# Performance work log

Hardware: AMD Instinct MI355X
Metric: run time of the kernel (lower is better)

## Reference

```python
import jax, jax.numpy as jnp
import numpy as np

B_ = 2; L_ = 4096; D_MODEL = 1024; D_INNER = 2048; D_STATE = 128
N_HEADS = 32; HEADDIM = 64; D_CONV = 4; CHUNK = 64
CONV_DIM = D_INNER + 2 * D_STATE
EPS = 1e-5


def silu(x):
    return x * jax.nn.sigmoid(x)


def segsum(x):
    # x: (..., T) -> (..., T, T) stable segment sums; exp() gives 1-semiseparable matrix
    T = x.shape[-1]
    xe = jnp.broadcast_to(x[..., None], x.shape + (T,))  # (..., T, T)
    lower = jnp.tril(jnp.ones((T, T), bool), -1)
    xs = jnp.cumsum(jnp.where(lower, xe, 0.0), axis=-2)
    incl = jnp.tril(jnp.ones((T, T), bool), 0)
    return jnp.where(incl, xs, -jnp.inf)


def ssd(x, A, Bm, Cm):
    # x: (b, l, h, p); A: (b, l, h); Bm/Cm: (b, l, n) (single shared head, as in module)
    b, l, h, p = x.shape
    c = l // CHUNK
    x = x.reshape(b, c, CHUNK, h, p)
    A = A.reshape(b, c, CHUNK, h).transpose(0, 3, 1, 2)  # (b, h, c, l)
    Bm = Bm.reshape(b, c, CHUNK, D_STATE)
    Cm = Cm.reshape(b, c, CHUNK, D_STATE)
    A_cumsum = jnp.cumsum(A, axis=-1)                    # (b, h, c, l)
    Lmat = jnp.exp(segsum(A))                            # (b, h, c, l, l)
    # intra-chunk (diagonal blocks)
    Y_diag = jnp.einsum('bcln,bcsn,bhcls,bcshp->bclhp', Cm, Bm, Lmat, x)
    # per-chunk states
    decay_states = jnp.exp(A_cumsum[:, :, :, -1:] - A_cumsum)  # (b, h, c, l)
    states = jnp.einsum('bcln,bhcl,bclhp->bchpn', Bm, decay_states, x)
    init = jnp.zeros_like(states[:, :1])
    states = jnp.concatenate([init, states], axis=1)     # (b, c+1, h, p, n)
    A_last = jnp.pad(A_cumsum[:, :, :, -1], ((0, 0), (0, 0), (1, 0)))  # (b, h, c+1)
    decay_chunk = jnp.exp(segsum(A_last))                # (b, h, c+1, c+1)
    new_states = jnp.einsum('bhzc,bchpn->bzhpn', decay_chunk, states)
    states_prev = new_states[:, :-1]                     # (b, c, h, p, n)
    state_decay_out = jnp.exp(A_cumsum)
    Y_off = jnp.einsum('bcln,bchpn,bhcl->bclhp', Cm, states_prev, state_decay_out)
    return (Y_diag + Y_off).reshape(b, l, h, p)


def setup_inputs() -> dict:
    key = jax.random.key(0)
    ks = jax.random.split(key, 9)
    u = jax.random.normal(ks[0], (B_, L_, D_MODEL), jnp.float32)
    W_in = jax.random.normal(ks[1], (2 * D_INNER + 2 * D_STATE + N_HEADS, D_MODEL), jnp.float32) * (D_MODEL ** -0.5)
    conv_w = jax.random.normal(ks[2], (CONV_DIM, 1, D_CONV), jnp.float32) * 0.2
    conv_b = jax.random.normal(ks[3], (CONV_DIM,), jnp.float32) * 0.02
    dt_bias = jax.random.normal(ks[4], (N_HEADS,), jnp.float32) * 0.1
    A_log = jnp.log(jax.random.uniform(ks[5], (N_HEADS,), jnp.float32, 1.0, 16.0))
    D_param = jax.random.normal(ks[6], (N_HEADS,), jnp.float32) * 0.5
    norm_w = jnp.ones((D_INNER,), jnp.float32)
    W_out = jax.random.normal(ks[7], (D_MODEL, D_INNER), jnp.float32) * (D_INNER ** -0.5)
    return dict(u=u, W_in=W_in, conv_w=conv_w, conv_b=conv_b, dt_bias=dt_bias,
                A_log=A_log, D_param=D_param, norm_w=norm_w, W_out=W_out)


def mamba_forward(u, W_in, conv_w, conv_b, dt_bias, A_log, D_param, norm_w, W_out):
    b, l, _ = u.shape
    zxbcdt = u @ W_in.T                                  # (b, l, 2*di+2*ds+h)
    z = zxbcdt[..., :D_INNER]
    xBC = zxbcdt[..., D_INNER:D_INNER + CONV_DIM]
    dt = zxbcdt[..., D_INNER + CONV_DIM:]
    dt = jax.nn.softplus(dt + dt_bias)                   # (b, l, h)
    # causal depthwise conv1d
    xc = jnp.transpose(xBC, (0, 2, 1))                   # (b, conv_dim, l)
    xc = jax.lax.conv_general_dilated(xc, conv_w, (1,), [(D_CONV - 1, 0)],
                                      feature_group_count=CONV_DIM,
                                      dimension_numbers=('NCH', 'OIH', 'NCH'))
    xc = xc + conv_b[None, :, None]
    xBC = silu(jnp.transpose(xc, (0, 2, 1)))             # (b, l, conv_dim)
    x = xBC[..., :D_INNER]
    Bc = xBC[..., D_INNER:D_INNER + D_STATE]
    Cc = xBC[..., D_INNER + D_STATE:]
    x = x.reshape(b, l, N_HEADS, HEADDIM)
    A = -jnp.exp(A_log)                                  # (h,)
    Y = ssd(x * dt[..., None], A * dt, Bc, Cc)           # (b, l, h, p)
    y = Y + x * D_param[:, None]
    y = y.reshape(b, l, D_INNER)
    # gated RMSNorm
    y = y * silu(z)
    y = y * jax.lax.rsqrt(jnp.mean(y * y, axis=-1, keepdims=True) + EPS) * norm_w
    return y @ W_out.T


def reference(u, W_in, conv_w, conv_b, dt_bias, A_log, D_param, norm_w, W_out):
    return mamba_forward(u, W_in, conv_w, conv_b, dt_bias, A_log, D_param, norm_w, W_out)
```

## Files before the change

### kernel.cpp

```cpp
#include <hip/hip_runtime.h>
#include <hip/hip_bf16.h>
#include <math.h>

#define B_    2
#define L_    4096
#define DM    1024
#define DI    2048
#define DS    128
#define NH    32
#define HD    64
#define CHUNK 64
#define NC    (L_/CHUNK)
#define CD    (DI + 2*DS)
#define ROWS  (B_*L_)
#define NOUT  (2*DI + 2*DS + NH)
#define NPAD2 4608

typedef __attribute__((ext_vector_type(4))) float f32x4;
typedef __attribute__((ext_vector_type(8))) __bf16 bf16x8;
typedef __attribute__((ext_vector_type(4))) short s16x4;
typedef __attribute__((ext_vector_type(8))) short s16x8;

__global__ __launch_bounds__(256) void k_f32_to_bf16(const float* __restrict__ s, __bf16* __restrict__ d, int n4) {
    int i = blockIdx.x * 256 + threadIdx.x;
    if (i < n4) {
        f32x4 v = *(const f32x4*)(s + (size_t)i * 4);
        s16x4 o;
#pragma unroll
        for (int q = 0; q < 4; q++) o[q] = __builtin_bit_cast(short, (__bf16)v[q]);
        *(s16x4*)(d + (size_t)i * 4) = o;
    }
}

__global__ __launch_bounds__(256) void k_convert_pad(const float* __restrict__ s, __bf16* __restrict__ d, int nsrc4, int ndst4) {
    int i = blockIdx.x * 256 + threadIdx.x;
    if (i < ndst4) {
        s16x4 o = {0, 0, 0, 0};
        if (i < nsrc4) {
            f32x4 v = *(const f32x4*)(s + (size_t)i * 4);
#pragma unroll
            for (int q = 0; q < 4; q++) o[q] = __builtin_bit_cast(short, (__bf16)v[q]);
        }
        *(s16x4*)(d + (size_t)i * 4) = o;
    }
}

__device__ __forceinline__ void stage_half(const __bf16* __restrict__ G, int ldg, int grow0, int kt,
                                           char* lds, int ldsoff, int tid, int wave) {
#pragma unroll
    for (int issue = 0; issue < 2; issue++) {
        int o   = issue * 8192 + tid * 16;
        int row = o >> 7;
        int cb  = (o & 127) ^ ((row & 7) << 4);
        const __bf16* src = G + (size_t)(grow0 + row) * ldg + kt + (cb >> 1);
        char* ldsbase = lds + ldsoff + issue * 8192 + wave * 1024;
        __builtin_amdgcn_global_load_lds((const __attribute__((address_space(1))) void*)src,
                                         (__attribute__((address_space(3))) void*)ldsbase,
                                         16, 0, 0);
    }
}

__device__ __forceinline__ bf16x8 rdfrag(const char* lds, int ldsoff, int r, int ks, int lane) {
    int logical = r * 128 + ks * 64 + ((lane >> 4) << 4);
    int phys    = logical ^ ((r & 7) << 4);
    return *(const bf16x8*)(lds + ldsoff + phys);
}

#define MFMA_CLUSTER(AF, BF, ACC)                                                         \
    __builtin_amdgcn_s_setprio(1);                                                       \
    _Pragma("unroll")                                                                    \
    for (int fm = 0; fm < 4; fm++)                                                       \
        _Pragma("unroll")                                                                \
        for (int fn = 0; fn < 2; fn++)                                                   \
            _Pragma("unroll")                                                            \
            for (int ks = 0; ks < 2; ks++)                                               \
                ACC[fm][fn] = __builtin_amdgcn_mfma_f32_16x16x32_bf16(AF[fm][ks], BF[fn][ks], ACC[fm][fn], 0, 0, 0); \
    __builtin_amdgcn_s_setprio(0);

__device__ __forceinline__ void gemm128x256_core(const __bf16* __restrict__ Ag, const __bf16* __restrict__ Bg,
                                                 int K, int m0, int n0, char* lds, f32x4 acc[4][4]) {
    const int tid = threadIdx.x, wave = tid >> 6, lane = tid & 63;
    const int wm = wave >> 2, wn = wave & 3, lrow = lane & 15;
    const int KT = K >> 6;
    const int brow = wn * 64;
    const int bhalf = 16384 + ((brow >> 7) << 14);
    const int brl = brow & 127;

    for (int t = 0; t < KT; t++) {
        const int kt = t << 6;
        stage_half(Ag, K, m0,       kt, lds, 0,     tid, wave);
        stage_half(Bg, K, n0,       kt, lds, 16384, tid, wave);
        stage_half(Bg, K, n0 + 128, kt, lds, 32768, tid, wave);
        asm volatile("s_waitcnt vmcnt(0)" ::: "memory");
        __builtin_amdgcn_s_barrier();
        bf16x8 a[4][2];
#pragma unroll
        for (int fm = 0; fm < 4; fm++)
#pragma unroll
            for (int ks = 0; ks < 2; ks++)
                a[fm][ks] = rdfrag(lds, 0, wm * 64 + fm * 16 + lrow, ks, lane);
        __builtin_amdgcn_s_setprio(1);
#pragma unroll
        for (int fn = 0; fn < 4; fn++) {
            bf16x8 b0 = rdfrag(lds, bhalf, brl + fn * 16 + lrow, 0, lane);
            bf16x8 b1 = rdfrag(lds, bhalf, brl + fn * 16 + lrow, 1, lane);
#pragma unroll
            for (int fm = 0; fm < 4; fm++) {
                acc[fm][fn] = __builtin_amdgcn_mfma_f32_16x16x32_bf16(a[fm][0], b0, acc[fm][fn], 0, 0, 0);
                acc[fm][fn] = __builtin_amdgcn_mfma_f32_16x16x32_bf16(a[fm][1], b1, acc[fm][fn], 0, 0, 0);
            }
        }
        __builtin_amdgcn_s_setprio(0);
        __builtin_amdgcn_s_barrier();
    }
}

__device__ __forceinline__ void gemm256x128_core(const __bf16* __restrict__ Ag, const __bf16* __restrict__ Bg,
                                                 int K, int m0, int n0, char* lds, f32x4 acc[8][2]) {
    const int tid = threadIdx.x, wave = tid >> 6, lane = tid & 63;
    const int wmq = wave >> 2, wnq = wave & 3, lrow = lane & 15;
    const int KT = K >> 6;
    const int aoff = wmq * 16384;

    auto stage_tile = [&](int t, int p) {
        const int kt = t << 6;
        stage_half(Ag, K, m0,       kt, lds, p * 49152,         tid, wave);
        stage_half(Ag, K, m0 + 128, kt, lds, p * 49152 + 16384, tid, wave);
        stage_half(Bg, K, n0,       kt, lds, p * 49152 + 32768, tid, wave);
    };
    stage_tile(0, 0);
    asm volatile("s_waitcnt vmcnt(0)" ::: "memory");
    __builtin_amdgcn_s_barrier();

    bf16x8 ra[4][2], rb[2][2];
#pragma unroll
    for (int fm = 0; fm < 4; fm++)
#pragma unroll
        for (int ks = 0; ks < 2; ks++)
            ra[fm][ks] = rdfrag(lds, aoff, fm * 16 + lrow, ks, lane);
#pragma unroll
    for (int fn = 0; fn < 2; fn++)
#pragma unroll
        for (int ks = 0; ks < 2; ks++)
            rb[fn][ks] = rdfrag(lds, 32768, wnq * 32 + fn * 16 + lrow, ks, lane);

    for (int t = 0; t < KT; t++) {
        const int p = t & 1, pn = p ^ 1;
        const bool dsg = (t + 1 < KT);
        if (dsg) {
            stage_half(Ag, K, m0,       (t + 1) << 6, lds, pn * 49152,         tid, wave);
            stage_half(Ag, K, m0 + 128, (t + 1) << 6, lds, pn * 49152 + 16384, tid, wave);
        }
        {
            f32x4 (*a0)[2] = &acc[0];
            MFMA_CLUSTER(ra, rb, a0);
        }
#pragma unroll
        for (int fm = 0; fm < 4; fm++)
#pragma unroll
            for (int ks = 0; ks < 2; ks++)
                ra[fm][ks] = rdfrag(lds, p * 49152 + aoff, 64 + fm * 16 + lrow, ks, lane);
        if (dsg) stage_half(Bg, K, n0, (t + 1) << 6, lds, pn * 49152 + 32768, tid, wave);
        {
            f32x4 (*a1)[2] = &acc[4];
            MFMA_CLUSTER(ra, rb, a1);
        }
        asm volatile("s_waitcnt vmcnt(0)" ::: "memory");
        __builtin_amdgcn_s_barrier();
        if (dsg) {
#pragma unroll
            for (int fm = 0; fm < 4; fm++)
#pragma unroll
                for (int ks = 0; ks < 2; ks++)
                    ra[fm][ks] = rdfrag(lds, pn * 49152 + aoff, fm * 16 + lrow, ks, lane);
#pragma unroll
            for (int fn = 0; fn < 2; fn++)
#pragma unroll
                for (int ks = 0; ks < 2; ks++)
                    rb[fn][ks] = rdfrag(lds, pn * 49152 + 32768, wnq * 32 + fn * 16 + lrow, ks, lane);
        }
    }
}

__global__ __launch_bounds__(512, 4) void k_gemm1(const __bf16* __restrict__ ubf, const __bf16* __restrict__ wibf,
                                                  __bf16* __restrict__ zbuf, __bf16* __restrict__ xbcraw,
                                                  float* __restrict__ dtbuf, const float* __restrict__ dt_bias) {
    extern __shared__ char lds[];
    f32x4 acc[4][4];
    f32x4 z4 = {0.f, 0.f, 0.f, 0.f};
#pragma unroll
    for (int i = 0; i < 4; i++)
#pragma unroll
        for (int j = 0; j < 4; j++) acc[i][j] = z4;

    int bid = blockIdx.x;
    int wg  = (bid & 7) * 144 + (bid >> 3);
    int m0  = (wg / 18) * 128;
    int n0  = (wg % 18) * 256;
    gemm128x256_core(ubf, wibf, DM, m0, n0, lds, acc);

    const int lane = threadIdx.x & 63, wave = threadIdx.x >> 6;
    const int wm = wave >> 2, wn = wave & 3;
    const int gm_base = m0 + wm * 64 + ((lane >> 4) << 2);
    const int gn_base = n0 + wn * 64 + (lane & 15);
#pragma unroll
    for (int fm = 0; fm < 4; fm++) {
        const int gmb = gm_base + fm * 16;
#pragma unroll
        for (int fn = 0; fn < 4; fn++) {
            const int gn = gn_base + fn * 16;
            if (gn < DI) {
#pragma unroll
                for (int r = 0; r < 4; r++)
                    zbuf[(size_t)(gmb + r) * DI + gn] = (__bf16)acc[fm][fn][r];
            } else if (gn < DI + CD) {
#pragma unroll
                for (int r = 0; r < 4; r++)
                    xbcraw[(size_t)(gmb + r) * CD + (gn - DI)] = (__bf16)acc[fm][fn][r];
            } else if (gn < NOUT) {
                const int hh = gn - (DI + CD);
                const float bb = dt_bias[hh];
#pragma unroll
                for (int r = 0; r < 4; r++) {
                    float x = acc[fm][fn][r] + bb;
                    float sp = (x > 20.f) ? x : log1pf(__expf(x));
                    dtbuf[(size_t)(gmb + r) * NH + hh] = sp;
                }
            }
        }
    }
}

__global__ __launch_bounds__(512, 2) void k_gemm2(const __bf16* __restrict__ ybf, const __bf16* __restrict__ wobf,
                                                  float* __restrict__ out) {
    extern __shared__ char lds[];
    f32x4 acc[8][2];
    f32x4 z4 = {0.f, 0.f, 0.f, 0.f};
#pragma unroll
    for (int i = 0; i < 8; i++)
#pragma unroll
        for (int j = 0; j < 2; j++) acc[i][j] = z4;

    int bid = blockIdx.x;
    int wg  = (bid & 7) * 32 + (bid >> 3);
    int m0  = (wg / 8) * 256;
    int n0  = (wg % 8) * 128;
    gemm256x128_core(ybf, wobf, DI, m0, n0, lds, acc);

    const int lane = threadIdx.x & 63, wave = threadIdx.x >> 6;
    const int wmq = wave >> 2, wnq = wave & 3;
#pragma unroll
    for (int fm = 0; fm < 8; fm++) {
        const int gmb = m0 + wmq * 128 + fm * 16 + ((lane >> 4) << 2);
#pragma unroll
        for (int fn = 0; fn < 2; fn++) {
            const int gn = n0 + wnq * 32 + fn * 16 + (lane & 15);
#pragma unroll
            for (int r = 0; r < 4; r++)
                out[(size_t)(gmb + r) * DM + gn] = acc[fm][fn][r];
        }
    }
}

__global__ __launch_bounds__(256) void k_conv(const __bf16* __restrict__ xbcraw, const float* __restrict__ conv_w,
                                              const float* __restrict__ conv_b, __bf16* __restrict__ xconv) {
    __shared__ float wsh[256 * 4];
    __shared__ float bsh[256];
    const int tid  = threadIdx.x;
    const int gsub = tid & 31;
    const int roct = tid >> 5;
    const int ch_base_blk = blockIdx.x * 256;
    *(f32x4*)&wsh[tid * 4] = *(const f32x4*)&conv_w[ch_base_blk * 4 + tid * 4];
    bsh[tid] = conv_b[ch_base_blk + tid];
    __syncthreads();

    const int ch0  = ch_base_blk + gsub * 8;
    const int row0 = (blockIdx.y * 8 + roct) * 8;
    const int l0   = row0 & (L_ - 1);
    const __bf16* src = xbcraw + (size_t)row0 * CD + ch0;

    s16x8 rr[11];
#pragma unroll
    for (int j = 0; j < 11; j++) {
        int ll = l0 - 3 + j;
        if (ll >= 0) rr[j] = *(const s16x8*)(src + (size_t)(j - 3) * CD);
        else         rr[j] = (s16x8){0, 0, 0, 0, 0, 0, 0, 0};
    }

    const int chl = gsub * 8;
    float w[8][4], bias[8];
#pragma unroll
    for (int j = 0; j < 8; j++) {
        bias[j] = bsh[chl + j];
#pragma unroll
        for (int k = 0; k < 4; k++) w[j][k] = wsh[(chl + j) * 4 + k];
    }

    __bf16* dst = xconv + (size_t)row0 * CD + ch0;
#pragma unroll
    for (int orow = 0; orow < 8; orow++) {
        float a[8];
#pragma unroll
        for (int j = 0; j < 8; j++) a[j] = bias[j];
#pragma unroll
        for (int k = 0; k < 4; k++) {
            s16x8 v = rr[orow + k];
#pragma unroll
            for (int j = 0; j < 8; j++)
                a[j] += w[j][k] * (float)__builtin_bit_cast(__bf16, (short)v[j]);
        }
        s16x8 o;
#pragma unroll
        for (int j = 0; j < 8; j++)
            o[j] = __builtin_bit_cast(short, (__bf16)(a[j] * __builtin_amdgcn_rcpf(1.f + __expf(-a[j]))));
        *(s16x8*)(dst + (size_t)orow * CD) = o;
    }
}

__global__ __launch_bounds__(256) void k_cbt(const __bf16* __restrict__ xconv, float* __restrict__ cbt) {
    const int c = blockIdx.x, b = blockIdx.y;
    const int tid = threadIdx.x, wv = tid >> 6, lane = tid & 63;
    const int lrow = lane & 15, lko = (lane >> 4) * 8;
    __shared__ __align__(16) __bf16 Csh[64 * 136];
    __shared__ __align__(16) __bf16 Bsh[64 * 136];
    const size_t rowbase = (size_t)b * L_ + c * CHUNK;
#pragma unroll
    for (int q = 0; q < 32; q++) {
        int i = q * 2 + (wv >> 1);
        int n = (wv & 1) * 64 + lane;
        const __bf16* base = xconv + (rowbase + i) * CD + DI;
        Bsh[i * 136 + n] = base[n];
        Csh[i * 136 + n] = base[DS + n];
    }
    __syncthreads();
    f32x4 acc[4];
    f32x4 z4 = {0.f, 0.f, 0.f, 0.f};
#pragma unroll
    for (int jt = 0; jt < 4; jt++) acc[jt] = z4;
#pragma unroll
    for (int ks = 0; ks < 4; ks++) {
        bf16x8 a = *(const bf16x8*)&Csh[(wv * 16 + lrow) * 136 + ks * 32 + lko];
#pragma unroll
        for (int jt = 0; jt < 4; jt++) {
            bf16x8 bb = *(const bf16x8*)&Bsh[(jt * 16 + lrow) * 136 + ks * 32 + lko];
            acc[jt] = __builtin_amdgcn_mfma_f32_16x16x32_bf16(a, bb, acc[jt], 0, 0, 0);
        }
    }
    float* o = cbt + (size_t)(b * NC + c) * 4096;
#pragma unroll
    for (int jt = 0; jt < 4; jt++)
#pragma unroll
        for (int r = 0; r < 4; r++) {
            int i = wv * 16 + (lane >> 4) * 4 + r;
            int j = jt * 16 + lrow;
            o[i * 64 + j] = acc[jt][r];
        }
}

__global__ __launch_bounds__(256) void k_ssd_a(const __bf16* __restrict__ xconv, const float* __restrict__ dtbuf,
                                               const float* __restrict__ cbt, const float* __restrict__ A_log,
                                               __bf16* __restrict__ ybuf, __bf16* __restrict__ states,
                                               float* __restrict__ asum, const float* __restrict__ D_param) {
    const int h = blockIdx.x, c = blockIdx.y, b = blockIdx.z;
    const int tid = threadIdx.x, wv = tid >> 6, lane = tid & 63;
    const int lrow = lane & 15, lko = (lane >> 4) * 8;
    __shared__ __align__(16) __bf16 xT[64 * 72];
    __shared__ __align__(16) __bf16 xsc[64 * 72];
    __shared__ __align__(16) __bf16 BT[128 * 72];
    __shared__ __align__(16) __bf16 Ms[64 * 72];
    __shared__ float dts[64], cum[64];

    const float Ah = -__expf(A_log[h]);
    const size_t rowbase = (size_t)b * L_ + c * CHUNK;

    float dtv = 0.f;
    if (wv == 0) { dtv = dtbuf[(rowbase + lane) * NH + h]; dts[lane] = dtv; }
#pragma unroll
    for (int q = 0; q < 16; q++) {
        int i = q * 4 + wv;
        xT[lane * 72 + i] = xconv[(rowbase + i) * CD + h * HD + lane];
    }
#pragma unroll
    for (int q = 0; q < 32; q++) {
        int i = q * 2 + (wv >> 1);
        int n = (wv & 1) * 64 + lane;
        BT[n * 72 + i] = xconv[(rowbase + i) * CD + DI + n];
    }
    if (wv == 0) {
        float v = Ah * dtv;
#pragma unroll
        for (int o = 1; o < 64; o <<= 1) { float t = __shfl_up(v, o); if (lane >= o) v += t; }
        cum[lane] = v;
        if (lane == 63) asum[(b * NC + c) * NH + h] = v;
    }
    __syncthreads();

    const float cum63 = cum[63];
    const float Dh = D_param[h];
    const float* cbt_bc = cbt + (size_t)(b * NC + c) * 4096;
#pragma unroll
    for (int q = 0; q < 16; q++) {
        int i = q * 4 + wv, j = lane;
        float cumi = cum[i];
        float m = 0.f;
        if (j <= i) m = cbt_bc[i * 64 + j] * __expf(cumi - cum[j]) * dts[j];
        if (j == i) m += Dh;
        Ms[i * 72 + j] = (__bf16)m;
        float dcfi = __expf(cum63 - cumi) * dts[i];
        xsc[lane * 72 + i] = (__bf16)((float)xT[lane * 72 + i] * dcfi);
    }
    __syncthreads();

    f32x4 z4 = {0.f, 0.f, 0.f, 0.f};
    {
        f32x4 accY[4];
#pragma unroll
        for (int pt = 0; pt < 4; pt++) accY[pt] = z4;
#pragma unroll
        for (int ks = 0; ks < 2; ks++) {
            bf16x8 a = *(const bf16x8*)&Ms[(wv * 16 + lrow) * 72 + ks * 32 + lko];
#pragma unroll
            for (int pt = 0; pt < 4; pt++) {
                bf16x8 bb = *(const bf16x8*)&xT[(pt * 16 + lrow) * 72 + ks * 32 + lko];
                accY[pt] = __builtin_amdgcn_mfma_f32_16x16x32_bf16(a, bb, accY[pt], 0, 0, 0);
            }
        }
#pragma unroll
        for (int pt = 0; pt < 4; pt++)
#pragma unroll
            for (int r = 0; r < 4; r++) {
                int i = wv * 16 + (lane >> 4) * 4 + r;
                int p = pt * 16 + lrow;
                ybuf[(rowbase + i) * DI + h * HD + p] = (__bf16)accY[pt][r];
            }
    }
    {
        f32x4 accS[8];
#pragma unroll
        for (int nt = 0; nt < 8; nt++) accS[nt] = z4;
#pragma unroll
        for (int ks = 0; ks < 2; ks++) {
            bf16x8 a = *(const bf16x8*)&xsc[(wv * 16 + lrow) * 72 + ks * 32 + lko];
#pragma unroll
            for (int nt = 0; nt < 8; nt++) {
                bf16x8 bb = *(const bf16x8*)&BT[(nt * 16 + lrow) * 72 + ks * 32 + lko];
                accS[nt] = __builtin_amdgcn_mfma_f32_16x16x32_bf16(a, bb, accS[nt], 0, 0, 0);
            }
        }
        __bf16* sp = states + ((size_t)(b * NC + c) * NH + h) * 8192;
#pragma unroll
        for (int nt = 0; nt < 8; nt++)
#pragma unroll
            for (int r = 0; r < 4; r++) {
                int p = wv * 16 + (lane >> 4) * 4 + r;
                int n = nt * 16 + lrow;
                sp[p * 128 + n] = (__bf16)accS[nt][r];
            }
    }
}

__global__ __launch_bounds__(256) void k_scan(__bf16* __restrict__ states, const float* __restrict__ asum) {
    const int seg = blockIdx.x, h = blockIdx.y, b = blockIdx.z;
    __shared__ float efs[NC];
    if (threadIdx.x < NC) efs[threadIdx.x] = __expf(asum[(b * NC + threadIdx.x) * NH + h]);
    __syncthreads();
    const int e0 = seg * 1024 + threadIdx.x * 4;
    __bf16* base = states + ((size_t)(b * NC) * NH + h) * 8192 + e0;
    const size_t cs = (size_t)NH * 8192;
    float S[4] = {0.f, 0.f, 0.f, 0.f};
    s16x4 r0 = *(const s16x4*)(base);
    s16x4 r1 = *(const s16x4*)(base + cs);
    s16x4 r2 = *(const s16x4*)(base + 2 * cs);
    s16x4 r3;
#define SCAN_STEP(RV, CC)                                                                  \
    {                                                                                      \
        s16x4 o; float e = efs[CC];                                                        \
        _Pragma("unroll")                                                                  \
        for (int q = 0; q < 4; q++) {                                                      \
            float t = (float)__builtin_bit_cast(__bf16, (short)RV[q]);                     \
            o[q] = __builtin_bit_cast(short, (__bf16)S[q]);                                \
            S[q] = e * S[q] + t;                                                           \
        }                                                                                  \
        *(s16x4*)(base + (size_t)(CC) * cs) = o;                                           \
    }
    for (int c = 0; c < NC; c += 4) {
        r3 = *(const s16x4*)(base + (size_t)(c + 3) * cs);
        SCAN_STEP(r0, c);
        if (c + 4 < NC) r0 = *(const s16x4*)(base + (size_t)(c + 4) * cs);
        SCAN_STEP(r1, c + 1);
        if (c + 5 < NC) r1 = *(const s16x4*)(base + (size_t)(c + 5) * cs);
        SCAN_STEP(r2, c + 2);
        if (c + 6 < NC) r2 = *(const s16x4*)(base + (size_t)(c + 6) * cs);
        SCAN_STEP(r3, c + 3);
    }
#undef SCAN_STEP
}

__global__ __launch_bounds__(256) void k_ssd_b(const __bf16* __restrict__ xconv, const float* __restrict__ dtbuf,
                                               const __bf16* __restrict__ states, const float* __restrict__ A_log,
                                               __bf16* __restrict__ ybuf) {
    const int h = blockIdx.x, c = blockIdx.y, b = blockIdx.z;
    const int tid = threadIdx.x, wv = tid >> 6, lane = tid & 63;
    const int lrow = lane & 15, lko = (lane >> 4) * 8;
    __shared__ __align__(16) __bf16 Csh[64 * 136];
    __shared__ __align__(16) __bf16 Sps[64 * 136];
    __shared__ float cum[64];

    const float Ah = -__expf(A_log[h]);
    const size_t rowbase = (size_t)b * L_ + c * CHUNK;
    const __bf16* sp = states + ((size_t)(b * NC + c) * NH + h) * 8192;
#pragma unroll
    for (int q = 0; q < 32; q++) {
        int i = q * 2 + (wv >> 1);
        int n = (wv & 1) * 64 + lane;
        Csh[i * 136 + n] = xconv[(rowbase + i) * CD + DI + DS + n];
        Sps[i * 136 + n] = sp[i * 128 + n];
    }
    if (wv == 0) {
        float v = Ah * dtbuf[(rowbase + lane) * NH + h];
#pragma unroll
        for (int o = 1; o < 64; o <<= 1) { float t = __shfl_up(v, o); if (lane >= o) v += t; }
        cum[lane] = v;
    }
    __syncthreads();

    f32x4 acc[4];
    f32x4 z4 = {0.f, 0.f, 0.f, 0.f};
#pragma unroll
    for (int pt = 0; pt < 4; pt++) acc[pt] = z4;
#pragma unroll
    for (int ks = 0; ks < 4; ks++) {
        bf16x8 a = *(const bf16x8*)&Csh[(wv * 16 + lrow) * 136 + ks * 32 + lko];
#pragma unroll
        for (int pt = 0; pt < 4; pt++) {
            bf16x8 bb = *(const bf16x8*)&Sps[(pt * 16 + lrow) * 136 + ks * 32 + lko];
            acc[pt] = __builtin_amdgcn_mfma_f32_16x16x32_bf16(a, bb, acc[pt], 0, 0, 0);
        }
    }
#pragma unroll
    for (int r = 0; r < 4; r++) {
        int i = wv * 16 + (lane >> 4) * 4 + r;
        float ef = __expf(cum[i]);
#pragma unroll
        for (int pt = 0; pt < 4; pt++) {
            size_t idx = (rowbase + i) * DI + h * HD + pt * 16 + lrow;
            float y0 = (float)ybuf[idx];
            ybuf[idx] = (__bf16)(y0 + ef * acc[pt][r]);
        }
    }
}

__global__ __launch_bounds__(256) void k_gate_norm(const __bf16* __restrict__ ybuf, const __bf16* __restrict__ zbuf,
                                                   const float* __restrict__ norm_w, __bf16* __restrict__ ybf) {
    const int r = blockIdx.x;
    const int tid = threadIdx.x;
    const int col0 = tid * 8;
    s16x8 y8 = *(const s16x8*)(ybuf + (size_t)r * DI + col0);
    s16x8 z8 = *(const s16x8*)(zbuf + (size_t)r * DI + col0);
    float v[8];
    float ss = 0.f;
#pragma unroll
    for (int q = 0; q < 8; q++) {
        float y = (float)__builtin_bit_cast(__bf16, (short)y8[q]);
        float z = (float)__builtin_bit_cast(__bf16, (short)z8[q]);
        float g = z * __builtin_amdgcn_rcpf(1.f + __expf(-z));
        v[q] = y * g;
        ss += v[q] * v[q];
    }
#pragma unroll
    for (int o = 32; o > 0; o >>= 1) ss += __shfl_down(ss, o);
    __shared__ float wsum[4];
    __shared__ float rmss;
    if ((tid & 63) == 0) wsum[tid >> 6] = ss;
    __syncthreads();
    if (tid == 0) {
        float t = wsum[0] + wsum[1] + wsum[2] + wsum[3];
        rmss = rsqrtf(t / (float)DI + 1e-5f);
    }
    __syncthreads();
    float rm = rmss;
    s16x8 o8;
#pragma unroll
    for (int q = 0; q < 8; q++)
        o8[q] = __builtin_bit_cast(short, (__bf16)(v[q] * rm * norm_w[col0 + q]));
    *(s16x8*)(ybf + (size_t)r * DI + col0) = o8;
}

extern "C" void kernel_launch(void* const* d_in, const int* in_sizes, int n_in,
                              void* d_out, int out_size, void* d_ws, size_t ws_size,
                              hipStream_t stream) {
    const float* u       = (const float*)d_in[0];
    const float* W_in    = (const float*)d_in[1];
    const float* conv_w  = (const float*)d_in[2];
    const float* conv_b  = (const float*)d_in[3];
    const float* dt_bias = (const float*)d_in[4];
    const float* A_log   = (const float*)d_in[5];
    const float* D_param = (const float*)d_in[6];
    const float* norm_w  = (const float*)d_in[7];
    const float* W_out   = (const float*)d_in[8];
    float* out = (float*)d_out;

    constexpr size_t OFF_WOBF  = 0;
    constexpr size_t OFF_ZBUF  = 4194304;
    constexpr size_t OFF_DT    = 37748736;
    constexpr size_t OFF_ASUM  = 38797312;
    constexpr size_t OFF_XCONV = 38813696;
    constexpr size_t OFF_CBT   = 76562432;
    constexpr size_t OFF_BIG   = 78659584;
    constexpr size_t NEED      = 145768448;
    if (ws_size < NEED) return;

    char* ws = (char*)d_ws;
    __bf16* wobf   = (__bf16*)(ws + OFF_WOBF);
    __bf16* zbuf   = (__bf16*)(ws + OFF_ZBUF);
    float*  dtbuf  = (float*) (ws + OFF_DT);
    float*  asum   = (float*) (ws + OFF_ASUM);
    __bf16* xconv  = (__bf16*)(ws + OFF_XCONV);
    float*  cbt    = (float*) (ws + OFF_CBT);
    __bf16* ubf    = (__bf16*)(ws + OFF_BIG);
    __bf16* wibf   = (__bf16*)(ws + OFF_BIG + 16777216);
    __bf16* xbcraw = (__bf16*)(ws + OFF_BIG + 16777216 + 9437184);
    __bf16* states = (__bf16*)(ws + OFF_BIG);
    __bf16* ybf    = (__bf16*)(ws + OFF_XCONV);
    __bf16* ybuf   = (__bf16*)d_out;

    (void)hipFuncSetAttribute((const void*)k_gemm1, hipFuncAttributeMaxDynamicSharedMemorySize, 49152);
    (void)hipFuncSetAttribute((const void*)k_gemm2, hipFuncAttributeMaxDynamicSharedMemorySize, 98304);

    k_f32_to_bf16<<<(ROWS * DM / 4 + 255) / 256, 256, 0, stream>>>(u, ubf, ROWS * DM / 4);
    k_convert_pad<<<(NPAD2 * DM / 4 + 255) / 256, 256, 0, stream>>>(W_in, wibf, NOUT * DM / 4, NPAD2 * DM / 4);
    k_f32_to_bf16<<<(DM * DI / 4 + 255) / 256, 256, 0, stream>>>(W_out, wobf, DM * DI / 4);

    k_gemm1<<<1152, 512, 49152, stream>>>(ubf, wibf, zbuf, xbcraw, dtbuf, dt_bias);
    k_conv<<<dim3(9, 128), 256, 0, stream>>>(xbcraw, conv_w, conv_b, xconv);
    k_cbt<<<dim3(NC, B_), 256, 0, stream>>>(xconv, cbt);
    k_ssd_a<<<dim3(NH, NC, B_), 256, 0, stream>>>(xconv, dtbuf, cbt, A_log, ybuf, states, asum, D_param);
    k_scan<<<dim3(8, NH, B_), 256, 0, stream>>>(states, asum);
    k_ssd_b<<<dim3(NH, NC, B_), 256, 0, stream>>>(xconv, dtbuf, states, A_log, ybuf);
    k_gate_norm<<<ROWS, 256, 0, stream>>>(ybuf, zbuf, norm_w, ybf);
    k_gemm2<<<256, 512, 98304, stream>>>(ybf, wobf, out);
}
```

Before: 308.7 us.

## Loop eight heads per block in SSD kernels to reuse B/C tiles; merge conversions

k_ssd_a and k_ssd_b now each process eight heads per block in a loop. The shared B (and C) chunk tile is staged into LDS once and reused across heads instead of being reloaded 32 times per chunk. The three fp32-to-bf16 conversion launches are merged into a single kernel to cut launch overhead. In exchange, the SSD grids shrink from 4096 to 512 blocks, and the per-head work inside each block is serialized with extra barriers, which lowers parallelism and latency hiding on a large GPU.

```diff
diff --git a/kernel.cpp b/kernel.cpp
--- a/kernel.cpp
+++ b/kernel.cpp
@@ -21,28 +21,33 @@
 typedef __attribute__((ext_vector_type(4))) short s16x4;
 typedef __attribute__((ext_vector_type(8))) short s16x8;
 
-__global__ __launch_bounds__(256) void k_f32_to_bf16(const float* __restrict__ s, __bf16* __restrict__ d, int n4) {
+__global__ __launch_bounds__(256) void k_convert_all(const float* __restrict__ u, const float* __restrict__ W_in,
+                                                     const float* __restrict__ W_out, __bf16* __restrict__ ubf,
+                                                     __bf16* __restrict__ wibf, __bf16* __restrict__ wobf) {
     int i = blockIdx.x * 256 + threadIdx.x;
-    if (i < n4) {
-        f32x4 v = *(const f32x4*)(s + (size_t)i * 4);
-        s16x4 o;
+    const int QU  = ROWS * DM / 4;
+    const int QWI = NPAD2 * DM / 4;
+    const int QWO = DM * DI / 4;
+    const float* s = nullptr;
+    __bf16* d;
+    bool zero = false;
+    if (i < QU) {
+        s = u + (size_t)i * 4; d = ubf + (size_t)i * 4;
+    } else if (i < QU + QWI) {
+        int j = i - QU;
+        d = wibf + (size_t)j * 4;
+        if (j < NOUT * DM / 4) s = W_in + (size_t)j * 4; else zero = true;
+    } else if (i < QU + QWI + QWO) {
+        int j = i - QU - QWI;
+        s = W_out + (size_t)j * 4; d = wobf + (size_t)j * 4;
+    } else return;
+    s16x4 o = {0, 0, 0, 0};
+    if (!zero) {
+        f32x4 v = *(const f32x4*)s;
 #pragma unroll
         for (int q = 0; q < 4; q++) o[q] = __builtin_bit_cast(short, (__bf16)v[q]);
-        *(s16x4*)(d + (size_t)i * 4) = o;
-    }
-}
-
-__global__ __launch_bounds__(256) void k_convert_pad(const float* __restrict__ s, __bf16* __restrict__ d, int nsrc4, int ndst4) {
-    int i = blockIdx.x * 256 + threadIdx.x;
-    if (i < ndst4) {
-        s16x4 o = {0, 0, 0, 0};
-        if (i < nsrc4) {
-            f32x4 v = *(const f32x4*)(s + (size_t)i * 4);
-#pragma unroll
-            for (int q = 0; q < 4; q++) o[q] = __builtin_bit_cast(short, (__bf16)v[q]);
-        }
-        *(s16x4*)(d + (size_t)i * 4) = o;
-    }
+    }
+    *(s16x4*)d = o;
 }
 
 __device__ __forceinline__ void stage_half(const __bf16* __restrict__ G, int ldg, int grow0, int kt,
@@ -361,7 +366,7 @@
                                                const float* __restrict__ cbt, const float* __restrict__ A_log,
                                                __bf16* __restrict__ ybuf, __bf16* __restrict__ states,
                                                float* __restrict__ asum, const float* __restrict__ D_param) {
-    const int h = blockIdx.x, c = blockIdx.y, b = blockIdx.z;
+    const int hg = blockIdx.x, c = blockIdx.y, b = blockIdx.z;
     const int tid = threadIdx.x, wv = tid >> 6, lane = tid & 63;
     const int lrow = lane & 15, lko = (lane >> 4) * 8;
     __shared__ __align__(16) __bf16 xT[64 * 72];
@@ -370,92 +375,96 @@
     __shared__ __align__(16) __bf16 Ms[64 * 72];
     __shared__ float dts[64], cum[64];
 
-    const float Ah = -__expf(A_log[h]);
     const size_t rowbase = (size_t)b * L_ + c * CHUNK;
-
-    float dtv = 0.f;
-    if (wv == 0) { dtv = dtbuf[(rowbase + lane) * NH + h]; dts[lane] = dtv; }
-#pragma unroll
-    for (int q = 0; q < 16; q++) {
-        int i = q * 4 + wv;
-        xT[lane * 72 + i] = xconv[(rowbase + i) * CD + h * HD + lane];
-    }
 #pragma unroll
     for (int q = 0; q < 32; q++) {
         int i = q * 2 + (wv >> 1);
         int n = (wv & 1) * 64 + lane;
         BT[n * 72 + i] = xconv[(rowbase + i) * CD + DI + n];
     }
-    if (wv == 0) {
-        float v = Ah * dtv;
-#pragma unroll
-        for (int o = 1; o < 64; o <<= 1) { float t = __shfl_up(v, o); if (lane >= o) v += t; }
-        cum[lane] = v;
-        if (lane == 63) asum[(b * NC + c) * NH + h] = v;
-    }
-    __syncthreads();
-
-    const float cum63 = cum[63];
-    const float Dh = D_param[h];
     const float* cbt_bc = cbt + (size_t)(b * NC + c) * 4096;
-#pragma unroll
-    for (int q = 0; q < 16; q++) {
-        int i = q * 4 + wv, j = lane;
-        float cumi = cum[i];
-        float m = 0.f;
-        if (j <= i) m = cbt_bc[i * 64 + j] * __expf(cumi - cum[j]) * dts[j];
-        if (j == i) m += Dh;
-        Ms[i * 72 + j] = (__bf16)m;
-        float dcfi = __expf(cum63 - cumi) * dts[i];
-        xsc[lane * 72 + i] = (__bf16)((float)xT[lane * 72 + i] * dcfi);
-    }
-    __syncthreads();
-
     f32x4 z4 = {0.f, 0.f, 0.f, 0.f};
-    {
-        f32x4 accY[4];
-#pragma unroll
-        for (int pt = 0; pt < 4; pt++) accY[pt] = z4;
-#pragma unroll
-        for (int ks = 0; ks < 2; ks++) {
-            bf16x8 a = *(const bf16x8*)&Ms[(wv * 16 + lrow) * 72 + ks * 32 + lko];
-#pragma unroll
-            for (int pt = 0; pt < 4; pt++) {
-                bf16x8 bb = *(const bf16x8*)&xT[(pt * 16 + lrow) * 72 + ks * 32 + lko];
-                accY[pt] = __builtin_amdgcn_mfma_f32_16x16x32_bf16(a, bb, accY[pt], 0, 0, 0);
+
+    for (int hh = 0; hh < 8; hh++) {
+        const int h = hg * 8 + hh;
+        const float Ah = -__expf(A_log[h]);
+        const float Dh = D_param[h];
+#pragma unroll
+        for (int q = 0; q < 16; q++) {
+            int i = q * 4 + wv;
+            xT[lane * 72 + i] = xconv[(rowbase + i) * CD + h * HD + lane];
+        }
+        if (wv == 0) {
+            float dtv = dtbuf[(rowbase + lane) * NH + h];
+            dts[lane] = dtv;
+            float v = Ah * dtv;
+#pragma unroll
+            for (int o = 1; o < 64; o <<= 1) { float t = __shfl_up(v, o); if (lane >= o) v += t; }
+            cum[lane] = v;
+            if (lane == 63) asum[(b * NC + c) * NH + h] = v;
+        }
+        __syncthreads();
+
+        const float cum63 = cum[63];
+#pragma unroll
+        for (int q = 0; q < 16; q++) {
+            int i = q * 4 + wv, j = lane;
+            float cumi = cum[i];
+            float m = 0.f;
+            if (j <= i) m = cbt_bc[i * 64 + j] * __expf(cumi - cum[j]) * dts[j];
+            if (j == i) m += Dh;
+            Ms[i * 72 + j] = (__bf16)m;
+            float dcfi = __expf(cum63 - cumi) * dts[i];
+            xsc[lane * 72 + i] = (__bf16)((float)xT[lane * 72 + i] * dcfi);
+        }
+        __syncthreads();
+
+        {
+            f32x4 accY[4];
+#pragma unroll
+            for (int pt = 0; pt < 4; pt++) accY[pt] = z4;
+#pragma unroll
+            for (int ks = 0; ks < 2; ks++) {
+                bf16x8 a = *(const bf16x8*)&Ms[(wv * 16 + lrow) * 72 + ks * 32 + lko];
+#pragma unroll
+                for (int pt = 0; pt < 4; pt++) {
+                    bf16x8 bb = *(const bf16x8*)&xT[(pt * 16 + lrow) * 72 + ks * 32 + lko];
+                    accY[pt] = __builtin_amdgcn_mfma_f32_16x16x32_bf16(a, bb, accY[pt], 0, 0, 0);
+                }
             }
-        }
-#pragma unroll
-        for (int pt = 0; pt < 4; pt++)
-#pragma unroll
-            for (int r = 0; r < 4; r++) {
-                int i = wv * 16 + (lane >> 4) * 4 + r;
-                int p = pt * 16 + lrow;
-                ybuf[(rowbase + i) * DI + h * HD + p] = (__bf16)accY[pt][r];
+#pragma unroll
+            for (int pt = 0; pt < 4; pt++)
+#pragma unroll
+                for (int r = 0; r < 4; r++) {
+                    int i = wv * 16 + (lane >> 4) * 4 + r;
+                    int p = pt * 16 + lrow;
+                    ybuf[(rowbase + i) * DI + h * HD + p] = (__bf16)accY[pt][r];
+                }
+        }
+        {
+            f32x4 accS[8];
+#pragma unroll
+            for (int nt = 0; nt < 8; nt++) accS[nt] = z4;
+#pragma unroll
+            for (int ks = 0; ks < 2; ks++) {
+                bf16x8 a = *(const bf16x8*)&xsc[(wv * 16 + lrow) * 72 + ks * 32 + lko];
+#pragma unroll
+                for (int nt = 0; nt < 8; nt++) {
+                    bf16x8 bb = *(const bf16x8*)&BT[(nt * 16 + lrow) * 72 + ks * 32 + lko];
+                    accS[nt] = __builtin_amdgcn_mfma_f32_16x16x32_bf16(a, bb, accS[nt], 0, 0, 0);
+                }
             }
-    }
-    {
-        f32x4 accS[8];
-#pragma unroll
-        for (int nt = 0; nt < 8; nt++) accS[nt] = z4;
-#pragma unroll
-        for (int ks = 0; ks < 2; ks++) {
-            bf16x8 a = *(const bf16x8*)&xsc[(wv * 16 + lrow) * 72 + ks * 32 + lko];
-#pragma unroll
-            for (int nt = 0; nt < 8; nt++) {
-                bf16x8 bb = *(const bf16x8*)&BT[(nt * 16 + lrow) * 72 + ks * 32 + lko];
-                accS[nt] = __builtin_amdgcn_mfma_f32_16x16x32_bf16(a, bb, accS[nt], 0, 0, 0);
-            }
-        }
-        __bf16* sp = states + ((size_t)(b * NC + c) * NH + h) * 8192;
-#pragma unroll
-        for (int nt = 0; nt < 8; nt++)
-#pragma unroll
-            for (int r = 0; r < 4; r++) {
-                int p = wv * 16 + (lane >> 4) * 4 + r;
-                int n = nt * 16 + lrow;
-                sp[p * 128 + n] = (__bf16)accS[nt][r];
-            }
+            __bf16* sp = states + ((size_t)(b * NC + c) * NH + h) * 8192;
+#pragma unroll
+            for (int nt = 0; nt < 8; nt++)
+#pragma unroll
+                for (int r = 0; r < 4; r++) {
+                    int p = wv * 16 + (lane >> 4) * 4 + r;
+                    int n = nt * 16 + lrow;
+                    sp[p * 128 + n] = (__bf16)accS[nt][r];
+                }
+        }
+        __syncthreads();
     }
 }
 
@@ -499,54 +508,64 @@
 __global__ __launch_bounds__(256) void k_ssd_b(const __bf16* __restrict__ xconv, const float* __restrict__ dtbuf,
                                                const __bf16* __restrict__ states, const float* __restrict__ A_log,
                                                __bf16* __restrict__ ybuf) {
-    const int h = blockIdx.x, c = blockIdx.y, b = blockIdx.z;
+    const int hg = blockIdx.x, c = blockIdx.y, b = blockIdx.z;
     const int tid = threadIdx.x, wv = tid >> 6, lane = tid & 63;
     const int lrow = lane & 15, lko = (lane >> 4) * 8;
     __shared__ __align__(16) __bf16 Csh[64 * 136];
     __shared__ __align__(16) __bf16 Sps[64 * 136];
     __shared__ float cum[64];
 
-    const float Ah = -__expf(A_log[h]);
     const size_t rowbase = (size_t)b * L_ + c * CHUNK;
-    const __bf16* sp = states + ((size_t)(b * NC + c) * NH + h) * 8192;
 #pragma unroll
     for (int q = 0; q < 32; q++) {
         int i = q * 2 + (wv >> 1);
         int n = (wv & 1) * 64 + lane;
         Csh[i * 136 + n] = xconv[(rowbase + i) * CD + DI + DS + n];
-        Sps[i * 136 + n] = sp[i * 128 + n];
-    }
-    if (wv == 0) {
-        float v = Ah * dtbuf[(rowbase + lane) * NH + h];
-#pragma unroll
-        for (int o = 1; o < 64; o <<= 1) { float t = __shfl_up(v, o); if (lane >= o) v += t; }
-        cum[lane] = v;
-    }
-    __syncthreads();
-
-    f32x4 acc[4];
+    }
     f32x4 z4 = {0.f, 0.f, 0.f, 0.f};
-#pragma unroll
-    for (int pt = 0; pt < 4; pt++) acc[pt] = z4;
-#pragma unroll
-    for (int ks = 0; ks < 4; ks++) {
-        bf16x8 a = *(const bf16x8*)&Csh[(wv * 16 + lrow) * 136 + ks * 32 + lko];
-#pragma unroll
-        for (int pt = 0; pt < 4; pt++) {
-            bf16x8 bb = *(const bf16x8*)&Sps[(pt * 16 + lrow) * 136 + ks * 32 + lko];
-            acc[pt] = __builtin_amdgcn_mfma_f32_16x16x32_bf16(a, bb, acc[pt], 0, 0, 0);
-        }
-    }
-#pragma unroll
-    for (int r = 0; r < 4; r++) {
-        int i = wv * 16 + (lane >> 4) * 4 + r;
-        float ef = __expf(cum[i]);
-#pragma unroll
-        for (int pt = 0; pt < 4; pt++) {
-            size_t idx = (rowbase + i) * DI + h * HD + pt * 16 + lrow;
-            float y0 = (float)ybuf[idx];
-            ybuf[idx] = (__bf16)(y0 + ef * acc[pt][r]);
-        }
+
+    for (int hh = 0; hh < 8; hh++) {
+        const int h = hg * 8 + hh;
+        const float Ah = -__expf(A_log[h]);
+        const __bf16* sp = states + ((size_t)(b * NC + c) * NH + h) * 8192;
+#pragma unroll
+        for (int q = 0; q < 32; q++) {
+            int i = q * 2 + (wv >> 1);
+            int n = (wv & 1) * 64 + lane;
+            Sps[i * 136 + n] = sp[i * 128 + n];
+        }
+        if (wv == 0) {
+            float v = Ah * dtbuf[(rowbase + lane) * NH + h];
+#pragma unroll
+            for (int o = 1; o < 64; o <<= 1) { float t = __shfl_up(v, o); if (lane >= o) v += t; }
+            cum[lane] = v;
+        }
+        __syncthreads();
+
+        f32x4 acc[4];
+#pragma unroll
+        for (int pt = 0; pt < 4; pt++) acc[pt] = z4;
+#pragma unroll
+        for (int ks = 0; ks < 4; ks++) {
+            bf16x8 a = *(const bf16x8*)&Csh[(wv * 16 + lrow) * 136 + ks * 32 + lko];
+#pragma unroll
+            for (int pt = 0; pt < 4; pt++) {
+                bf16x8 bb = *(const bf16x8*)&Sps[(pt * 16 + lrow) * 136 + ks * 32 + lko];
+                acc[pt] = __builtin_amdgcn_mfma_f32_16x16x32_bf16(a, bb, acc[pt], 0, 0, 0);
+            }
+        }
+#pragma unroll
+        for (int r = 0; r < 4; r++) {
+            int i = wv * 16 + (lane >> 4) * 4 + r;
+            float ef = __expf(cum[i]);
+#pragma unroll
+            for (int pt = 0; pt < 4; pt++) {
+                size_t idx = (rowbase + i) * DI + h * HD + pt * 16 + lrow;
+                float y0 = (float)ybuf[idx];
+                ybuf[idx] = (__bf16)(y0 + ef * acc[pt][r]);
+            }
+        }
+        __syncthreads();
     }
 }
 
@@ -627,16 +646,15 @@
     (void)hipFuncSetAttribute((const void*)k_gemm1, hipFuncAttributeMaxDynamicSharedMemorySize, 49152);
     (void)hipFuncSetAttribute((const void*)k_gemm2, hipFuncAttributeMaxDynamicSharedMemorySize, 98304);
 
-    k_f32_to_bf16<<<(ROWS * DM / 4 + 255) / 256, 256, 0, stream>>>(u, ubf, ROWS * DM / 4);
-    k_convert_pad<<<(NPAD2 * DM / 4 + 255) / 256, 256, 0, stream>>>(W_in, wibf, NOUT * DM / 4, NPAD2 * DM / 4);
-    k_f32_to_bf16<<<(DM * DI / 4 + 255) / 256, 256, 0, stream>>>(W_out, wobf, DM * DI / 4);
+    constexpr int QTOT = ROWS * DM / 4 + NPAD2 * DM / 4 + DM * DI / 4;
+    k_convert_all<<<(QTOT + 255) / 256, 256, 0, stream>>>(u, W_in, W_out, ubf, wibf, wobf);
 
     k_gemm1<<<1152, 512, 49152, stream>>>(ubf, wibf, zbuf, xbcraw, dtbuf, dt_bias);
     k_conv<<<dim3(9, 128), 256, 0, stream>>>(xbcraw, conv_w, conv_b, xconv);
     k_cbt<<<dim3(NC, B_), 256, 0, stream>>>(xconv, cbt);
-    k_ssd_a<<<dim3(NH, NC, B_), 256, 0, stream>>>(xconv, dtbuf, cbt, A_log, ybuf, states, asum, D_param);
+    k_ssd_a<<<dim3(4, NC, B_), 256, 0, stream>>>(xconv, dtbuf, cbt, A_log, ybuf, states, asum, D_param);
     k_scan<<<dim3(8, NH, B_), 256, 0, stream>>>(states, asum);
-    k_ssd_b<<<dim3(NH, NC, B_), 256, 0, stream>>>(xconv, dtbuf, states, A_log, ybuf);
+    k_ssd_b<<<dim3(4, NC, B_), 256, 0, stream>>>(xconv, dtbuf, states, A_log, ybuf);
     k_gate_norm<<<ROWS, 256, 0, stream>>>(ybuf, zbuf, norm_w, ybf);
     k_gemm2<<<256, 512, 98304, stream>>>(ybf, wobf, out);
 }
```

Measured after the change: 369.4 us. +19.7%, slower.
